# Optimization experiments

Measured on AMD Instinct MI355X. Metric: run time of the kernel, lower is better.

The kernel has to match this reference:

```python
import jax, jax.numpy as jnp
import numpy as np

N_ATOMS = 100000
N_BONDS = 200000
N_MOLS = 2000
ATOMS_PER_MOL = 50
ATOM_FDIM = 18
BOND_FDIM = 5
MAX_NB = 15
HIDDEN = 128
DEPTH = 6


def setup_inputs() -> dict:
    key = jax.random.key(0)
    ks = jax.random.split(key, 8)
    fatoms = jax.random.uniform(ks[0], (N_ATOMS, ATOM_FDIM), dtype=jnp.float32)
    fbonds = jax.random.uniform(ks[1], (N_BONDS, ATOM_FDIM + BOND_FDIM), dtype=jnp.float32)
    agraph = jax.random.randint(ks[2], (N_ATOMS, MAX_NB), 0, N_BONDS, dtype=jnp.int32)
    bgraph = jax.random.randint(ks[3], (N_BONDS, MAX_NB), 0, N_BONDS, dtype=jnp.int32)
    scope_start = (jnp.arange(N_MOLS, dtype=jnp.int32) * ATOMS_PER_MOL)
    scope_len = jnp.full((N_MOLS,), ATOMS_PER_MOL, dtype=jnp.int32)
    # parameters (torch Linear: y = x @ W.T; store as [in, out])
    s_i = 1.0 / np.sqrt(ATOM_FDIM + BOND_FDIM)
    s_h = 1.0 / np.sqrt(HIDDEN)
    s_o = 1.0 / np.sqrt(ATOM_FDIM + HIDDEN)
    W_i = jax.random.uniform(ks[4], (ATOM_FDIM + BOND_FDIM, HIDDEN), jnp.float32, -s_i, s_i)
    W_h = jax.random.uniform(ks[5], (HIDDEN, HIDDEN), jnp.float32, -s_h, s_h)
    W_o = jax.random.uniform(ks[6], (ATOM_FDIM + HIDDEN, HIDDEN), jnp.float32, -s_o, s_o)
    b_o = jax.random.uniform(ks[7], (HIDDEN,), jnp.float32, -s_o, s_o)
    return {"fatoms": fatoms, "fbonds": fbonds, "agraph": agraph, "bgraph": bgraph,
            "scope_start": scope_start, "scope_len": scope_len,
            "W_i": W_i, "W_h": W_h, "W_o": W_o, "b_o": b_o}


def reference(fatoms, fbonds, agraph, bgraph, scope_start, scope_len, W_i, W_h, W_o, b_o):
    binput = fbonds @ W_i                      # [E, H]
    message = jax.nn.relu(binput)
    for _ in range(DEPTH - 1):
        nei = jnp.take(message, bgraph, axis=0).sum(axis=1)   # gather [E,MAX_NB,H] -> sum
        message = jax.nn.relu(binput + nei @ W_h)
    nei_a = jnp.take(message, agraph, axis=0).sum(axis=1)     # [N, H]
    ainput = jnp.concatenate([fatoms, nei_a], axis=1)         # [N, ATOM_FDIM+H]
    atom_hiddens = jax.nn.relu(ainput @ W_o + b_o)            # [N, H]
    # ragged scope-based mean pooling (segment mean)
    n_mols = scope_len.shape[0]
    seg = jnp.repeat(jnp.arange(n_mols, dtype=jnp.int32), scope_len,
                     total_repeat_length=atom_hiddens.shape[0])
    sums = jax.ops.segment_sum(atom_hiddens, seg, num_segments=n_mols)
    mol_vecs = sums / scope_len[:, None].astype(atom_hiddens.dtype)
    return mol_vecs
```

## Files before the change

### kernel.cpp

```cpp
#include <hip/hip_runtime.h>

#define EDGES 200000
#define NATOMS 100000
#define NMOLS 2000
#define H 128
#define MAXNB 15
#define AFD 18
#define INFD 23
#define LROW 136


typedef unsigned short bf16s;
typedef unsigned char u8;
typedef __attribute__((ext_vector_type(8))) short short8;
typedef __attribute__((ext_vector_type(4))) float f32x4;
typedef __attribute__((ext_vector_type(2))) float f32x2;

__device__ inline float bf2f(bf16s u) {
  union { unsigned int i; float f; } c; c.i = ((unsigned int)u) << 16; return c.f;
}
__device__ inline bf16s f2bf(float f) {
  union { float f; unsigned int i; } c; c.f = f;
  unsigned int lsb = (c.i >> 16) & 1u;
  c.i += 0x7fffu + lsb;
  return (bf16s)(c.i >> 16);
}
__device__ inline f32x2 bfpair(unsigned int u) {
  union { unsigned int i; float f; } lo, hi;
  lo.i = u << 16; hi.i = u & 0xffff0000u;
  return (f32x2){lo.f, hi.f};
}
__device__ inline unsigned int pack2(f32x2 v) {
  return (unsigned int)f2bf(fmaxf(v.x, 0.f)) |
         ((unsigned int)f2bf(fmaxf(v.y, 0.f)) << 16);
}
__device__ inline void store4(bf16s* p, const float v[4]) {
  ushort4 t; t.x = f2bf(v[0]); t.y = f2bf(v[1]); t.z = f2bf(v[2]); t.w = f2bf(v[3]);
  *(ushort4*)p = t;
}

__global__ __launch_bounds__(256) void k_wt(
    const float* __restrict__ Wh, const float* __restrict__ Wo,
    bf16s* __restrict__ wt_h, bf16s* __restrict__ wt_o) {
  const float* S = blockIdx.x ? (Wo + AFD * H) : Wh;
  bf16s* D = blockIdx.x ? wt_o : wt_h;
  for (int i = threadIdx.x; i < H * H; i += 256) {
    int k = i >> 7, n = i & 127;
    D[n * H + k] = f2bf(S[i]);
  }
}

template <int OUT_Q>
__device__ inline void mfma_epi(const bf16s* Aw, const bf16s* __restrict__ Wt,
                                void* __restrict__ PoutV, bf16s* __restrict__ Sout,
                                int ebase, int lane) {
  const int mm = lane & 15;
  const int quad = lane >> 4;
  const bf16s* Wp = Wt + (size_t)mm * H + quad * 8;
  const int rbase = ebase + quad * 4;
  f32x4 acc[2][4];
#pragma unroll
  for (int h = 0; h < 2; ++h)
#pragma unroll
    for (int i = 0; i < 4; ++i) acc[h][i] = (f32x4){0.f, 0.f, 0.f, 0.f};
#pragma unroll
  for (int kk = 0; kk < 4; ++kk) {
    short8 af = *(const short8*)&Aw[mm * LROW + quad * 8 + kk * 32];
#pragma unroll
    for (int h = 0; h < 2; ++h)
#pragma unroll
      for (int nt = 0; nt < 4; ++nt) {
        short8 bfr = *(const short8*)(Wp + (size_t)((h * 4 + nt) * 16) * H + kk * 32);
        acc[h][nt] = __builtin_amdgcn_mfma_f32_16x16x32_bf16(af, bfr, acc[h][nt], 0, 0, 0);
      }
  }
  if constexpr (OUT_Q) {
    u8* P8 = (u8*)PoutV;
    float m[4][4];
#pragma unroll
    for (int i = 0; i < 4; ++i)
#pragma unroll
      for (int b = 0; b < 4; ++b) m[i][b] = 0.f;
#pragma unroll
    for (int h = 0; h < 2; ++h)
#pragma unroll
      for (int nt = 0; nt < 4; ++nt) {
        const int b = h * 2 + (nt >> 1);
#pragma unroll
        for (int i = 0; i < 4; ++i) m[i][b] = fmaxf(m[i][b], fabsf(acc[h][nt][i]));
      }
#pragma unroll
    for (int w = 1; w < 16; w <<= 1)
#pragma unroll
      for (int i = 0; i < 4; ++i)
#pragma unroll
        for (int b = 0; b < 4; ++b)
          m[i][b] = fmaxf(m[i][b], __shfl_xor(m[i][b], w, 16));
    float rs[4][4];
    unsigned short sbits[4][4];
#pragma unroll
    for (int i = 0; i < 4; ++i)
#pragma unroll
      for (int b = 0; b < 4; ++b) {
        bf16s sb = f2bf(m[i][b] * (1.f / 127.f));
        float sd = bf2f(sb);
        rs[i][b] = sd > 0.f ? 1.f / sd : 0.f;
        sbits[i][b] = sb;
      }
    if (mm == 0) {
#pragma unroll
      for (int i = 0; i < 4; ++i) {
        ushort4 sv;
        sv.x = sbits[i][0]; sv.y = sbits[i][1];
        sv.z = sbits[i][2]; sv.w = sbits[i][3];
        *(ushort4*)&Sout[(size_t)(rbase + i) * 4] = sv;
      }
    }
#pragma unroll
    for (int h = 0; h < 2; ++h)
#pragma unroll
      for (int nt = 0; nt < 4; ++nt) {
        const int b = h * 2 + (nt >> 1);
#pragma unroll
        for (int i = 0; i < 4; ++i) {
          float q = fminf(fmaxf(acc[h][nt][i] * rs[i][b] + 128.5f, 0.f), 255.f);
          P8[(size_t)(rbase + i) * H + (h * 4 + nt) * 16 + mm] = (u8)(unsigned)q;
        }
      }
  } else {
    bf16s* Pout = (bf16s*)PoutV;
#pragma unroll
    for (int h = 0; h < 2; ++h)
#pragma unroll
      for (int nt = 0; nt < 4; ++nt)
#pragma unroll
        for (int i = 0; i < 4; ++i)
          Pout[(size_t)(rbase + i) * H + (h * 4 + nt) * 16 + mm] = f2bf(acc[h][nt][i]);
  }
}

__global__ __launch_bounds__(256) void k_binput_gemm(
    const float* __restrict__ fbonds, const float* __restrict__ Wi,
    const bf16s* __restrict__ wt_h, bf16s* __restrict__ binput,
    bf16s* __restrict__ P1) {
  __shared__ float Wl[INFD * H];
  __shared__ bf16s Am[4][16 * LROW];
  const int tid = threadIdx.x;
  for (int i = tid; i < INFD * H; i += 256) Wl[i] = Wi[i];
  __syncthreads();
  const int wave = tid >> 6;
  const int lane = tid & 63;
  bf16s* Aw = Am[wave];
  const int ebase = (blockIdx.x * 4 + wave) * 16;
  const int sub = lane >> 5;
  const int col = lane & 31;
  for (int r = 0; r < 8; ++r) {
    const int erow = r * 2 + sub;
    const int e = ebase + erow;
    const float* fb = &fbonds[(size_t)e * INFD];
    float acc[4] = {0.f, 0.f, 0.f, 0.f};
#pragma unroll
    for (int k = 0; k < INFD; ++k) {
      float f = fb[k];
      float4 w = *(const float4*)&Wl[k * H + col * 4];
      acc[0] = fmaf(f, w.x, acc[0]); acc[1] = fmaf(f, w.y, acc[1]);
      acc[2] = fmaf(f, w.z, acc[2]); acc[3] = fmaf(f, w.w, acc[3]);
    }
    store4(&binput[(size_t)e * H + col * 4], acc);
    ushort4 mq;
    mq.x = f2bf(fmaxf(acc[0], 0.f)); mq.y = f2bf(fmaxf(acc[1], 0.f));
    mq.z = f2bf(fmaxf(acc[2], 0.f)); mq.w = f2bf(fmaxf(acc[3], 0.f));
    *(ushort4*)&Aw[erow * LROW + col * 4] = mq;
  }
  asm volatile("s_waitcnt lgkmcnt(0)" ::: "memory");
  mfma_epi<0>(Aw, wt_h, P1, nullptr, ebase, lane);
}

template <int TBL_Q, int OUT_Q>
__global__ __launch_bounds__(128, 4) void k_fused(
    const int* __restrict__ bgraph, const void* __restrict__ Pv,
    const bf16s* __restrict__ Sin, const bf16s* __restrict__ binput,
    const bf16s* __restrict__ Wt, void* __restrict__ Pout,
    bf16s* __restrict__ Sout) {
  __shared__ bf16s Am[2][16 * LROW];
  const int tid = threadIdx.x;
  const int wave = tid >> 6;
  const int lane = tid & 63;
  bf16s* Aw = Am[wave];
  const int ebase = (blockIdx.x * 2 + wave) * 16;

  const int sub = lane >> 4;
  const int col = lane & 15;
#pragma unroll
  for (int it = 0; it < 4; ++it) {
    const int erow = it * 4 + sub;
    const int e = ebase + erow;
    int idx[MAXNB];
#pragma unroll
    for (int j = 0; j < MAXNB; ++j) idx[j] = bgraph[(size_t)e * MAXNB + j];

    uint4 bi = *(const uint4*)&binput[(size_t)e * H + col * 8];
    f32x2 acc0 = bfpair(bi.x), acc1 = bfpair(bi.y);
    f32x2 acc2 = bfpair(bi.z), acc3 = bfpair(bi.w);

    if constexpr (TBL_Q) {
      const u8* P = (const u8*)Pv;
      uint2 t[MAXNB];
      float s[MAXNB];
#pragma unroll
      for (int j = 0; j < MAXNB; ++j) {
        t[j] = *(const uint2*)&P[(size_t)idx[j] * H + col * 8];
        s[j] = bf2f(Sin[(size_t)idx[j] * 4 + (col >> 2)]);
      }
      float ssum = 0.f;
#pragma unroll
      for (int j = 0; j < MAXNB; ++j) ssum += s[j];
#pragma unroll
      for (int j = 0; j < MAXNB; ++j) {
        const unsigned x = t[j].x, y = t[j].y;
        const float sj = s[j];
        acc0.x = fmaf(sj, (float)(x & 0xffu), acc0.x);
        acc0.y = fmaf(sj, (float)((x >> 8) & 0xffu), acc0.y);
        acc1.x = fmaf(sj, (float)((x >> 16) & 0xffu), acc1.x);
        acc1.y = fmaf(sj, (float)(x >> 24), acc1.y);
        acc2.x = fmaf(sj, (float)(y & 0xffu), acc2.x);
        acc2.y = fmaf(sj, (float)((y >> 8) & 0xffu), acc2.y);
        acc3.x = fmaf(sj, (float)((y >> 16) & 0xffu), acc3.x);
        acc3.y = fmaf(sj, (float)(y >> 24), acc3.y);
      }
      const float off = 128.f * ssum;
      acc0.x -= off; acc0.y -= off; acc1.x -= off; acc1.y -= off;
      acc2.x -= off; acc2.y -= off; acc3.x -= off; acc3.y -= off;
    } else {
      const bf16s* P = (const bf16s*)Pv;
      uint4 t[MAXNB];
#pragma unroll
      for (int j = 0; j < MAXNB; ++j)
        t[j] = *(const uint4*)&P[(size_t)idx[j] * H + col * 8];
#pragma unroll
      for (int j = 0; j < MAXNB; ++j) {
        acc0 += bfpair(t[j].x); acc1 += bfpair(t[j].y);
        acc2 += bfpair(t[j].z); acc3 += bfpair(t[j].w);
      }
    }
    uint4 o;
    o.x = pack2(acc0); o.y = pack2(acc1); o.z = pack2(acc2); o.w = pack2(acc3);
    *(uint4*)&Aw[erow * LROW + col * 8] = o;
  }
  asm volatile("s_waitcnt lgkmcnt(0)" ::: "memory");
  mfma_epi<OUT_Q>(Aw, Wt, Pout, Sout, ebase, lane);
}

__global__ __launch_bounds__(256, 4) void k_atoms(
    const float* __restrict__ fatoms, const int* __restrict__ agraph,
    const bf16s* __restrict__ msgWo, const float* __restrict__ Wo,
    const float* __restrict__ bo, bf16s* __restrict__ atomh) {
  __shared__ float Wl[AFD * H];
  const int tid = threadIdx.x;
  for (int i = tid; i < AFD * H; i += 256) Wl[i] = Wo[i];
  __syncthreads();
  const int col = tid & 15;
  const int a = blockIdx.x * 16 + (tid >> 4);
  int idx[MAXNB];
#pragma unroll
  for (int j = 0; j < MAXNB; ++j) idx[j] = agraph[(size_t)a * MAXNB + j];
  uint4 t[MAXNB];
#pragma unroll
  for (int j = 0; j < MAXNB; ++j)
    t[j] = *(const uint4*)&msgWo[(size_t)idx[j] * H + col * 8];
  float4 b0 = ((const float4*)bo)[col * 2];
  float4 b1 = ((const float4*)bo)[col * 2 + 1];
  f32x2 acc0 = (f32x2){b0.x, b0.y}, acc1 = (f32x2){b0.z, b0.w};
  f32x2 acc2 = (f32x2){b1.x, b1.y}, acc3 = (f32x2){b1.z, b1.w};
#pragma unroll
  for (int k = 0; k < AFD; ++k) {
    float f = fatoms[(size_t)a * AFD + k];
    float4 w0 = *(const float4*)&Wl[k * H + col * 8];
    float4 w1 = *(const float4*)&Wl[k * H + col * 8 + 4];
    acc0.x = fmaf(f, w0.x, acc0.x); acc0.y = fmaf(f, w0.y, acc0.y);
    acc1.x = fmaf(f, w0.z, acc1.x); acc1.y = fmaf(f, w0.w, acc1.y);
    acc2.x = fmaf(f, w1.x, acc2.x); acc2.y = fmaf(f, w1.y, acc2.y);
    acc3.x = fmaf(f, w1.z, acc3.x); acc3.y = fmaf(f, w1.w, acc3.y);
  }
#pragma unroll
  for (int j = 0; j < MAXNB; ++j) {
    acc0 += bfpair(t[j].x); acc1 += bfpair(t[j].y);
    acc2 += bfpair(t[j].z); acc3 += bfpair(t[j].w);
  }
  uint4 o;
  o.x = pack2(acc0); o.y = pack2(acc1); o.z = pack2(acc2); o.w = pack2(acc3);
  *(uint4*)&atomh[(size_t)a * H + col * 8] = o;
}

__global__ void k_pool(const bf16s* __restrict__ atomh,
                       const int* __restrict__ sstart, const int* __restrict__ slen,
                       float* __restrict__ out) {
  const int m = blockIdx.x;
  const int c = threadIdx.x;
  const int s = sstart[m];
  const int L = slen[m];
  float sum = 0.f;
  for (int i = 0; i < L; ++i) sum += bf2f(atomh[(size_t)(s + i) * H + c]);
  out[m * H + c] = sum / (float)L;
}

extern "C" void kernel_launch(void* const* d_in, const int* in_sizes, int n_in,
                              void* d_out, int out_size, void* d_ws, size_t ws_size,
                              hipStream_t stream) {
  const float* fatoms = (const float*)d_in[0];
  const float* fbonds = (const float*)d_in[1];
  const int* agraph = (const int*)d_in[2];
  const int* bgraph = (const int*)d_in[3];
  const int* sstart = (const int*)d_in[4];
  const int* slen = (const int*)d_in[5];
  const float* Wi = (const float*)d_in[6];
  const float* Wh = (const float*)d_in[7];
  const float* Wo = (const float*)d_in[8];
  const float* bo = (const float*)d_in[9];
  float* out = (float*)d_out;

  const size_t EH = (size_t)EDGES * H;
  char* W = (char*)d_ws;
  bf16s* binput = (bf16s*)W;
  bf16s* B1 = (bf16s*)(W + 2 * EH);
  bf16s* BB = (bf16s*)(W + 4 * EH);
  u8*    QA = (u8*)(W + 2 * EH);
  bf16s* SA = (bf16s*)(W + 3 * EH);
  u8*    QB = (u8*)(W + 4 * EH);
  bf16s* SB = (bf16s*)(W + 5 * EH);
  bf16s* atomh = (bf16s*)W;
  bf16s* wt_h = (bf16s*)d_out;
  bf16s* wt_o = wt_h + H * H;

  k_wt<<<2, 256, 0, stream>>>(Wh, Wo, wt_h, wt_o);
  k_binput_gemm<<<EDGES / 64, 256, 0, stream>>>(fbonds, Wi, wt_h, binput, B1);
  k_fused<0, 0><<<EDGES / 32, 128, 0, stream>>>(bgraph, B1, nullptr, binput, wt_h, BB, nullptr);
  k_fused<0, 1><<<EDGES / 32, 128, 0, stream>>>(bgraph, BB, nullptr, binput, wt_h, QA, SA);
  k_fused<1, 1><<<EDGES / 32, 128, 0, stream>>>(bgraph, QA, SA, binput, wt_h, QB, SB);
  k_fused<1, 1><<<EDGES / 32, 128, 0, stream>>>(bgraph, QB, SB, binput, wt_h, QA, SA);
  k_fused<1, 0><<<EDGES / 32, 128, 0, stream>>>(bgraph, QA, SA, binput, wt_o, BB, nullptr);
  k_atoms<<<NATOMS / 16, 256, 0, stream>>>(fatoms, agraph, BB, Wo, bo, atomh);
  k_pool<<<NMOLS, H, 0, stream>>>(atomh, sstart, slen, out);
}
```

Baseline: 843.5 us.

## Store binput as fp8, quantize final message to int8, use DPP max-reduce

Stores the bond input projection as packed fp8 and converts it back with the hardware pk_f32_fp8 instruction, halving the bytes read per edge in every message-passing step. The last message layer now emits per-row-block int8 values with bf16 scales, and the atom kernel dequantizes them while gathering, cutting the bytes moved by the agraph gather. The per-row max reduction in the quantizing epilogue uses DPP row operations instead of xor shuffles. Together these trade more precision loss (fp8 binput, int8 final messages) for less memory traffic in a bandwidth-bound gather workload.

Measured after the change: 801.3 us. -5.0%, faster.

```diff
diff --git a/kernel.cpp b/kernel.cpp
--- a/kernel.cpp
+++ b/kernel.cpp
@@ -34,9 +34,23 @@
   return (unsigned int)f2bf(fmaxf(v.x, 0.f)) |
          ((unsigned int)f2bf(fmaxf(v.y, 0.f)) << 16);
 }
-__device__ inline void store4(bf16s* p, const float v[4]) {
-  ushort4 t; t.x = f2bf(v[0]); t.y = f2bf(v[1]); t.z = f2bf(v[2]); t.w = f2bf(v[3]);
-  *(ushort4*)p = t;
+__device__ inline unsigned int pack4_fp8(float a, float b, float c, float d) {
+  int lo = __builtin_amdgcn_cvt_pk_fp8_f32(a, b, 0, false);
+  int full = __builtin_amdgcn_cvt_pk_fp8_f32(c, d, lo, true);
+  return (unsigned int)full;
+}
+#define DPPMAX_STEP(m, CTRL)                                                   \
+  {                                                                            \
+    int _t = __builtin_amdgcn_update_dpp(                                      \
+        0, __builtin_bit_cast(int, m), CTRL, 0xf, 0xf, false);                 \
+    m = fmaxf(m, __builtin_bit_cast(float, _t));                               \
+  }
+__device__ inline float dpp_max16(float m) {
+  DPPMAX_STEP(m, 0x121);
+  DPPMAX_STEP(m, 0x122);
+  DPPMAX_STEP(m, 0x124);
+  DPPMAX_STEP(m, 0x128);
+  return m;
 }
 
 __global__ __launch_bounds__(256) void k_wt(
@@ -90,12 +104,9 @@
         for (int i = 0; i < 4; ++i) m[i][b] = fmaxf(m[i][b], fabsf(acc[h][nt][i]));
       }
 #pragma unroll
-    for (int w = 1; w < 16; w <<= 1)
-#pragma unroll
-      for (int i = 0; i < 4; ++i)
-#pragma unroll
-        for (int b = 0; b < 4; ++b)
-          m[i][b] = fmaxf(m[i][b], __shfl_xor(m[i][b], w, 16));
+    for (int i = 0; i < 4; ++i)
+#pragma unroll
+      for (int b = 0; b < 4; ++b) m[i][b] = dpp_max16(m[i][b]);
     float rs[4][4];
     unsigned short sbits[4][4];
 #pragma unroll
@@ -141,7 +152,7 @@
 
 __global__ __launch_bounds__(256) void k_binput_gemm(
     const float* __restrict__ fbonds, const float* __restrict__ Wi,
-    const bf16s* __restrict__ wt_h, bf16s* __restrict__ binput,
+    const bf16s* __restrict__ wt_h, u8* __restrict__ binput8,
     bf16s* __restrict__ P1) {
   __shared__ float Wl[INFD * H];
   __shared__ bf16s Am[4][16 * LROW];
@@ -166,7 +177,8 @@
       acc[0] = fmaf(f, w.x, acc[0]); acc[1] = fmaf(f, w.y, acc[1]);
       acc[2] = fmaf(f, w.z, acc[2]); acc[3] = fmaf(f, w.w, acc[3]);
     }
-    store4(&binput[(size_t)e * H + col * 4], acc);
+    *(unsigned int*)&binput8[(size_t)e * H + col * 4] =
+        pack4_fp8(acc[0], acc[1], acc[2], acc[3]);
     ushort4 mq;
     mq.x = f2bf(fmaxf(acc[0], 0.f)); mq.y = f2bf(fmaxf(acc[1], 0.f));
     mq.z = f2bf(fmaxf(acc[2], 0.f)); mq.w = f2bf(fmaxf(acc[3], 0.f));
@@ -179,7 +191,7 @@
 template <int TBL_Q, int OUT_Q>
 __global__ __launch_bounds__(128, 4) void k_fused(
     const int* __restrict__ bgraph, const void* __restrict__ Pv,
-    const bf16s* __restrict__ Sin, const bf16s* __restrict__ binput,
+    const bf16s* __restrict__ Sin, const u8* __restrict__ binput8,
     const bf16s* __restrict__ Wt, void* __restrict__ Pout,
     bf16s* __restrict__ Sout) {
   __shared__ bf16s Am[2][16 * LROW];
@@ -199,9 +211,11 @@
 #pragma unroll
     for (int j = 0; j < MAXNB; ++j) idx[j] = bgraph[(size_t)e * MAXNB + j];
 
-    uint4 bi = *(const uint4*)&binput[(size_t)e * H + col * 8];
-    f32x2 acc0 = bfpair(bi.x), acc1 = bfpair(bi.y);
-    f32x2 acc2 = bfpair(bi.z), acc3 = bfpair(bi.w);
+    uint2 bi = *(const uint2*)&binput8[(size_t)e * H + col * 8];
+    f32x2 acc0 = __builtin_amdgcn_cvt_pk_f32_fp8(bi.x, false);
+    f32x2 acc1 = __builtin_amdgcn_cvt_pk_f32_fp8(bi.x, true);
+    f32x2 acc2 = __builtin_amdgcn_cvt_pk_f32_fp8(bi.y, false);
+    f32x2 acc3 = __builtin_amdgcn_cvt_pk_f32_fp8(bi.y, true);
 
     if constexpr (TBL_Q) {
       const u8* P = (const u8*)Pv;
@@ -253,8 +267,9 @@
 
 __global__ __launch_bounds__(256, 4) void k_atoms(
     const float* __restrict__ fatoms, const int* __restrict__ agraph,
-    const bf16s* __restrict__ msgWo, const float* __restrict__ Wo,
-    const float* __restrict__ bo, bf16s* __restrict__ atomh) {
+    const u8* __restrict__ msgQ, const bf16s* __restrict__ msgS,
+    const float* __restrict__ Wo, const float* __restrict__ bo,
+    bf16s* __restrict__ atomh) {
   __shared__ float Wl[AFD * H];
   const int tid = threadIdx.x;
   for (int i = tid; i < AFD * H; i += 256) Wl[i] = Wo[i];
@@ -264,10 +279,13 @@
   int idx[MAXNB];
 #pragma unroll
   for (int j = 0; j < MAXNB; ++j) idx[j] = agraph[(size_t)a * MAXNB + j];
-  uint4 t[MAXNB];
-#pragma unroll
-  for (int j = 0; j < MAXNB; ++j)
-    t[j] = *(const uint4*)&msgWo[(size_t)idx[j] * H + col * 8];
+  uint2 t[MAXNB];
+  float s[MAXNB];
+#pragma unroll
+  for (int j = 0; j < MAXNB; ++j) {
+    t[j] = *(const uint2*)&msgQ[(size_t)idx[j] * H + col * 8];
+    s[j] = bf2f(msgS[(size_t)idx[j] * 4 + (col >> 2)]);
+  }
   float4 b0 = ((const float4*)bo)[col * 2];
   float4 b1 = ((const float4*)bo)[col * 2 + 1];
   f32x2 acc0 = (f32x2){b0.x, b0.y}, acc1 = (f32x2){b0.z, b0.w};
@@ -282,11 +300,25 @@
     acc2.x = fmaf(f, w1.x, acc2.x); acc2.y = fmaf(f, w1.y, acc2.y);
     acc3.x = fmaf(f, w1.z, acc3.x); acc3.y = fmaf(f, w1.w, acc3.y);
   }
+  float ssum = 0.f;
+#pragma unroll
+  for (int j = 0; j < MAXNB; ++j) ssum += s[j];
 #pragma unroll
   for (int j = 0; j < MAXNB; ++j) {
-    acc0 += bfpair(t[j].x); acc1 += bfpair(t[j].y);
-    acc2 += bfpair(t[j].z); acc3 += bfpair(t[j].w);
-  }
+    const unsigned x = t[j].x, y = t[j].y;
+    const float sj = s[j];
+    acc0.x = fmaf(sj, (float)(x & 0xffu), acc0.x);
+    acc0.y = fmaf(sj, (float)((x >> 8) & 0xffu), acc0.y);
+    acc1.x = fmaf(sj, (float)((x >> 16) & 0xffu), acc1.x);
+    acc1.y = fmaf(sj, (float)(x >> 24), acc1.y);
+    acc2.x = fmaf(sj, (float)(y & 0xffu), acc2.x);
+    acc2.y = fmaf(sj, (float)((y >> 8) & 0xffu), acc2.y);
+    acc3.x = fmaf(sj, (float)((y >> 16) & 0xffu), acc3.x);
+    acc3.y = fmaf(sj, (float)(y >> 24), acc3.y);
+  }
+  const float off = 128.f * ssum;
+  acc0.x -= off; acc0.y -= off; acc1.x -= off; acc1.y -= off;
+  acc2.x -= off; acc2.y -= off; acc3.x -= off; acc3.y -= off;
   uint4 o;
   o.x = pack2(acc0); o.y = pack2(acc1); o.z = pack2(acc2); o.w = pack2(acc3);
   *(uint4*)&atomh[(size_t)a * H + col * 8] = o;
@@ -321,7 +353,7 @@
 
   const size_t EH = (size_t)EDGES * H;
   char* W = (char*)d_ws;
-  bf16s* binput = (bf16s*)W;
+  u8*    binput8 = (u8*)W;
   bf16s* B1 = (bf16s*)(W + 2 * EH);
   bf16s* BB = (bf16s*)(W + 4 * EH);
   u8*    QA = (u8*)(W + 2 * EH);
@@ -333,12 +365,12 @@
   bf16s* wt_o = wt_h + H * H;
 
   k_wt<<<2, 256, 0, stream>>>(Wh, Wo, wt_h, wt_o);
-  k_binput_gemm<<<EDGES / 64, 256, 0, stream>>>(fbonds, Wi, wt_h, binput, B1);
-  k_fused<0, 0><<<EDGES / 32, 128, 0, stream>>>(bgraph, B1, nullptr, binput, wt_h, BB, nullptr);
-  k_fused<0, 1><<<EDGES / 32, 128, 0, stream>>>(bgraph, BB, nullptr, binput, wt_h, QA, SA);
-  k_fused<1, 1><<<EDGES / 32, 128, 0, stream>>>(bgraph, QA, SA, binput, wt_h, QB, SB);
-  k_fused<1, 1><<<EDGES / 32, 128, 0, stream>>>(bgraph, QB, SB, binput, wt_h, QA, SA);
-  k_fused<1, 0><<<EDGES / 32, 128, 0, stream>>>(bgraph, QA, SA, binput, wt_o, BB, nullptr);
-  k_atoms<<<NATOMS / 16, 256, 0, stream>>>(fatoms, agraph, BB, Wo, bo, atomh);
+  k_binput_gemm<<<EDGES / 64, 256, 0, stream>>>(fbonds, Wi, wt_h, binput8, B1);
+  k_fused<0, 0><<<EDGES / 32, 128, 0, stream>>>(bgraph, B1, nullptr, binput8, wt_h, BB, nullptr);
+  k_fused<0, 1><<<EDGES / 32, 128, 0, stream>>>(bgraph, BB, nullptr, binput8, wt_h, QA, SA);
+  k_fused<1, 1><<<EDGES / 32, 128, 0, stream>>>(bgraph, QA, SA, binput8, wt_h, QB, SB);
+  k_fused<1, 1><<<EDGES / 32, 128, 0, stream>>>(bgraph, QB, SB, binput8, wt_h, QA, SA);
+  k_fused<1, 1><<<EDGES / 32, 128, 0, stream>>>(bgraph, QA, SA, binput8, wt_o, QB, SB);
+  k_atoms<<<NATOMS / 16, 256, 0, stream>>>(fatoms, agraph, QB, SB, Wo, bo, atomh);
   k_pool<<<NMOLS, H, 0, stream>>>(atomh, sstart, slen, out);
 }
```
